# Kernel tuning notes

Measured on AMD Instinct MI355X. Metric: run time of the kernel, lower is better.

Reference implementation:

```python
import jax, jax.numpy as jnp
import numpy as np

N_NODES = 100000
N_EDGES = 1600000
IN_DIM = 128
OUT_DIM = 128


def setup_inputs() -> dict:
    key = jax.random.key(0)
    k1, k2, k3, k4, k5 = jax.random.split(key, 5)
    x = jax.random.normal(k1, (N_NODES, IN_DIM), dtype=jnp.float32)
    edge_src = jax.random.randint(k2, (N_EDGES,), 0, N_NODES, dtype=jnp.int32)
    edge_dst = jax.random.randint(k3, (N_EDGES,), 0, N_NODES, dtype=jnp.int32)
    # nn.Linear(in_dim*2, out_dim): W stored here as [2*in_dim, out_dim] (already transposed)
    W = jax.random.normal(k4, (2 * IN_DIM, OUT_DIM), dtype=jnp.float32) * (1.0 / np.sqrt(2 * IN_DIM))
    b = jax.random.normal(k5, (OUT_DIM,), dtype=jnp.float32) * 0.01
    return {"x": x, "edge_src": edge_src, "edge_dst": edge_dst, "W": W, "b": b}


def reference(x, edge_src, edge_dst, W, b):
    # adj_mean @ x  ==  mean over neighbors: sum_j x[src_j] into row dst_j, / deg(dst)
    n = x.shape[0]
    deg = jax.ops.segment_sum(jnp.ones_like(edge_dst, dtype=x.dtype), edge_dst, num_segments=n)
    deg = jnp.maximum(deg, 1.0)  # rows with no neighbors -> zero vector (0/1)
    neigh = jax.ops.segment_sum(x[edge_src], edge_dst, num_segments=n) / deg[:, None]
    # concat([x, neigh], dim=1) then Linear
    out = jnp.concatenate([x, neigh], axis=1) @ W + b
    return out
```

## Files before the change

### kernel.cpp

```cpp
#include <hip/hip_runtime.h>

#define IN_DIM 128
#define OUT_DIM 128
#define PADCAP 1792
#define EPB 8192

typedef short bf16x8 __attribute__((ext_vector_type(8)));
typedef float f32x4 __attribute__((ext_vector_type(4)));
typedef float f32x2 __attribute__((ext_vector_type(2)));
typedef unsigned int u32x4 __attribute__((ext_vector_type(4)));

__device__ __forceinline__ unsigned short f2bf(float f) {
    union { float f; unsigned int u; } v; v.f = f;
    unsigned int u = v.u;
    u += 0x7FFFu + ((u >> 16) & 1u);
    return (unsigned short)(u >> 16);
}

__global__ __launch_bounds__(256) void prep_kernel(const float* __restrict__ x,
                                                   unsigned char* __restrict__ xq,
                                                   const float* __restrict__ W,
                                                   unsigned short* __restrict__ WF,
                                                   int* __restrict__ cursor,
                                                   int nN, int total8, int nconv, int nb) {
    const int b = blockIdx.x;
    const int t = threadIdx.x;
    if (b < nconv) {
        int i = b * 256 + t;
        if (i >= total8) return;
        const float4* p = (const float4*)x + (size_t)i * 2;
        float4 v0 = p[0], v1 = p[1];
        int w0 = 0, w1 = 0;
        w0 = __builtin_amdgcn_cvt_pk_fp8_f32(v0.x, v0.y, w0, false);
        w0 = __builtin_amdgcn_cvt_pk_fp8_f32(v0.z, v0.w, w0, true);
        w1 = __builtin_amdgcn_cvt_pk_fp8_f32(v1.x, v1.y, w1, false);
        w1 = __builtin_amdgcn_cvt_pk_fp8_f32(v1.z, v1.w, w1, true);
        uint2 o; o.x = (unsigned int)w0; o.y = (unsigned int)w1;
        int node = i >> 4, oct = i & 15;
        int q = oct >> 2, o8 = oct & 3;
        *(uint2*)(xq + (size_t)q * (nN + 1) * 32 + (size_t)node * 32 + o8 * 8) = o;
    } else if (b < nconv + 16) {
        int tt = (b - nconv) * 256 + t;
        int frag = tt >> 6, lane = tt & 63;
        int f = frag >> 3, c = frag & 7;
        int col = c * 16 + (lane & 15);
        int kbase = f * 32 + (lane >> 4) * 8;
        bf16x8 h;
#pragma unroll
        for (int i = 0; i < 8; i++)
            h[i] = (short)f2bf(W[(size_t)(kbase + i) * OUT_DIM + col]);
        *(bf16x8*)(WF + (size_t)tt * 8) = h;
    } else if (b == nconv + 16) {
        if (t < 32) {
            int q = t >> 3, o = t & 7;
            *(unsigned int*)(xq + (size_t)q * (nN + 1) * 32 + (size_t)nN * 32 + o * 4) = 0u;
        }
    } else {
        int i = (b - nconv - 17) * 256 + t;
        if (i < nb) cursor[i] = i * PADCAP;
    }
}

__global__ __launch_bounds__(1024) void place_kernel(const int* __restrict__ src,
                                                     const int* __restrict__ dst,
                                                     int* __restrict__ cursor,
                                                     unsigned int* __restrict__ csr_packed,
                                                     int nE, int nb) {
    __shared__ int lcnt[2048];
    __shared__ int lbase[2048];
    const int t = threadIdx.x;
    for (int i = t; i < nb; i += 1024) lcnt[i] = 0;
    __syncthreads();
    const int e0 = blockIdx.x * EPB;
    unsigned int meta[EPB / 1024];
#pragma unroll
    for (int k = 0; k < EPB / 1024; k++) {
        int e = e0 + k * 1024 + t;
        if (e < nE) {
            int d = dst[e];
            int bk = d >> 6, dl = d & 63;
            int r = atomicAdd(&lcnt[bk], 1);
            meta[k] = ((unsigned)bk << 20) | ((unsigned)dl << 14) | (unsigned)r;
        } else meta[k] = 0xFFFFFFFFu;
    }
    __syncthreads();
    for (int i = t; i < nb; i += 1024) {
        int c = lcnt[i];
        lbase[i] = c ? atomicAdd(&cursor[i], c) : 0;
    }
    __syncthreads();
#pragma unroll
    for (int k = 0; k < EPB / 1024; k++) {
        if (meta[k] != 0xFFFFFFFFu) {
            int e = e0 + k * 1024 + t;
            unsigned int m = meta[k];
            int bk = m >> 20, dl = (m >> 14) & 63, r = m & 0x3FFF;
            csr_packed[lbase[bk] + r] = ((unsigned)dl << 17) | (unsigned)src[e];
        }
    }
}

__global__ __launch_bounds__(256) void sort_kernel(unsigned int* __restrict__ csr_packed,
                                                   int* __restrict__ cursor,
                                                   unsigned int* __restrict__ rowinfo,
                                                   int nN, int nb) {
    __shared__ int bcnt[64];
    __shared__ int bpst[64];
    __shared__ int s_npad;
    __shared__ unsigned int sorted[PADCAP];
    const int b = blockIdx.x;
    const int t = threadIdx.x;
    const int lane = t & 63;
    const int wave = t >> 6;
    const size_t e0 = (size_t)b * PADCAP;
    int n = cursor[b] - (int)(b * PADCAP);
    if (n > PADCAP) n = PADCAP;

    const unsigned int sentinel = (unsigned)nN << 5;
    if (t < 64) bcnt[t] = 0;
#pragma unroll
    for (int k = 0; k < 7; k++) sorted[k * 256 + t] = sentinel;
    __syncthreads();

    unsigned int pk[7]; int rk[7];
#pragma unroll
    for (int k = 0; k < 7; k++) {
        int idx = k * 256 + t;
        if (idx < n) {
            unsigned int p = csr_packed[e0 + idx];
            pk[k] = p;
            rk[k] = atomicAdd(&bcnt[(p >> 17) & 63], 1);
        } else pk[k] = 0xFFFFFFFFu;
    }
    __syncthreads();

    if (wave == 0) {
        int dg = bcnt[lane];
        int pl = (dg + 7) & ~7;
        int s = pl;
#pragma unroll
        for (int off = 1; off < 64; off <<= 1) {
            int u = __shfl_up(s, off);
            if (lane >= off) s += u;
        }
        bpst[lane] = s - pl;
        if (lane == 63) s_npad = s;
        unsigned key = ((unsigned)dg << 6) | (unsigned)lane;
#pragma unroll
        for (int k = 2; k <= 64; k <<= 1) {
#pragma unroll
            for (int j = k >> 1; j > 0; j >>= 1) {
                unsigned other = __shfl_xor(key, j);
                bool lower = (lane & j) == 0;
                bool asc   = (lane & k) == 0;
                unsigned mn = min(key, other), mx = max(key, other);
                key = (lower == asc) ? mn : mx;
            }
        }
        int rowid = key & 63;
        int deg2  = key >> 6;
        rowinfo[b * 64 + lane] = (unsigned)bpst[rowid] | ((unsigned)deg2 << 11)
                               | ((unsigned)rowid << 21);
    }
    __syncthreads();

#pragma unroll
    for (int k = 0; k < 7; k++) {
        if (pk[k] != 0xFFFFFFFFu) {
            int dl = (pk[k] >> 17) & 63;
            sorted[bpst[dl] + rk[k]] = (pk[k] & 0x1FFFFu) << 5;
        }
    }
    __syncthreads();

    const int npadtot = s_npad;
#pragma unroll
    for (int k = 0; k < 7; k++) {
        int idx = k * 256 + t;
        if (idx < npadtot) csr_packed[e0 + idx] = sorted[idx];
    }
    if (t == 0) cursor[b] = npadtot;
}

__global__ __launch_bounds__(256, 8) void qgather_kernel(const unsigned char* __restrict__ xq,
                                                         const unsigned int* __restrict__ csr_packed,
                                                         const unsigned int* __restrict__ rowinfo,
                                                         const int* __restrict__ cursor,
                                                         unsigned short* __restrict__ neigh,
                                                         int nN, int nb) {
    __shared__ unsigned int el[PADCAP];
    __shared__ int bst[64];
    __shared__ int bdg[64];
    __shared__ int brw[64];

    const int bid = blockIdx.x;
    const int xcd = bid & 7;
    const int quarter = xcd & 3;
    const int bucket = (bid >> 3) * 2 + (xcd >> 2);
    if (bucket >= nb) return;

    const int t = threadIdx.x;
    const int lane = t & 63;
    const int wave = t >> 6;

    if (t < 64) {
        unsigned int ri = rowinfo[bucket * 64 + t];
        bst[t] = (int)(ri & 0x7FFu);
        bdg[t] = (int)((ri >> 11) & 0x3FFu);
        brw[t] = (int)((ri >> 21) & 63u);
    }
    __syncthreads();
    const size_t e0 = (size_t)bucket * PADCAP;
    const int npad = cursor[bucket];
    for (int idx = t; idx < npad; idx += 256) el[idx] = csr_packed[e0 + idx];
    __syncthreads();

    const int g = lane >> 2;
    const int c = lane & 3;
    const unsigned char* plane = xq + (size_t)quarter * (nN + 1) * 32 + c * 8;
    const int qoff = quarter * 32;

    const int r  = wave * 16 + g;
    const int st = bst[r];
    const int dg = bdg[r];
    const int pl = (dg + 7) & ~7;
    const unsigned int* ep = el + st;

    f32x2 a0{0.f, 0.f}, a1{0.f, 0.f}, a2{0.f, 0.f}, a3{0.f, 0.f};
    for (int j = 0; j < pl; j += 8) {
#pragma unroll
        for (int u = 0; u < 8; u++) {
            unsigned int s = ep[j + ((u + g) & 7)];
            uint2 v = *(const uint2*)(plane + s);
            f32x2 p;
            p = __builtin_amdgcn_cvt_pk_f32_fp8(v.x, false); a0 += p;
            p = __builtin_amdgcn_cvt_pk_f32_fp8(v.x, true);  a1 += p;
            p = __builtin_amdgcn_cvt_pk_f32_fp8(v.y, false); a2 += p;
            p = __builtin_amdgcn_cvt_pk_f32_fp8(v.y, true);  a3 += p;
        }
    }
    const float rd = 1.0f / (float)((dg > 0) ? dg : 1);
    a0 *= rd; a1 *= rd; a2 *= rd; a3 *= rd;
    unsigned int w0, w1, w2, w3;
    asm("v_cvt_pk_bf16_f32 %0, %1, %2" : "=v"(w0) : "v"(a0.x), "v"(a0.y));
    asm("v_cvt_pk_bf16_f32 %0, %1, %2" : "=v"(w1) : "v"(a1.x), "v"(a1.y));
    asm("v_cvt_pk_bf16_f32 %0, %1, %2" : "=v"(w2) : "v"(a2.x), "v"(a2.y));
    asm("v_cvt_pk_bf16_f32 %0, %1, %2" : "=v"(w3) : "v"(a3.x), "v"(a3.y));
    u32x4 o = {w0, w1, w2, w3};
    const int row = bucket * 64 + brw[r];
    *(u32x4*)(neigh + (size_t)row * IN_DIM + qoff + c * 8) = o;
}

__global__ __launch_bounds__(256, 6) void gemm_kernel(const float* __restrict__ x,
                                                      const unsigned short* __restrict__ neigh,
                                                      const unsigned short* __restrict__ WF,
                                                      const float* __restrict__ bias,
                                                      float* __restrict__ out, int nN) {
    const int t = threadIdx.x;
    const int lane = t & 63;
    const int wave = t >> 6;
    const int row0 = blockIdx.x * 64;

    f32x4 acc[8];
#pragma unroll
    for (int c = 0; c < 8; c++) acc[c] = f32x4{0.f, 0.f, 0.f, 0.f};

    const int arow = wave * 16 + (lane & 15);
    const int koff = (lane >> 4) * 8;
    const int rowc = min(row0 + arow, nN - 1);
    const float*          xrow = x     + (size_t)rowc * IN_DIM;
    const unsigned short* nrow = neigh + (size_t)rowc * IN_DIM;

#pragma unroll
    for (int f = 0; f < 8; f++) {
        bf16x8 af;
        if (f < 4) {
            const float* px = xrow + f * 32 + koff;
            float4 v0 = *(const float4*)px;
            float4 v1 = *(const float4*)(px + 4);
            unsigned int r0, r1, r2, r3;
            asm("v_cvt_pk_bf16_f32 %0, %1, %2" : "=v"(r0) : "v"(v0.x), "v"(v0.y));
            asm("v_cvt_pk_bf16_f32 %0, %1, %2" : "=v"(r1) : "v"(v0.z), "v"(v0.w));
            asm("v_cvt_pk_bf16_f32 %0, %1, %2" : "=v"(r2) : "v"(v1.x), "v"(v1.y));
            asm("v_cvt_pk_bf16_f32 %0, %1, %2" : "=v"(r3) : "v"(v1.z), "v"(v1.w));
            union { unsigned int u[4]; bf16x8 v; } cv;
            cv.u[0] = r0; cv.u[1] = r1; cv.u[2] = r2; cv.u[3] = r3;
            af = cv.v;
        } else {
            af = *(const bf16x8*)(nrow + (f - 4) * 32 + koff);
        }
#pragma unroll
        for (int c = 0; c < 8; c++) {
            bf16x8 bf = *(const bf16x8*)(WF + ((size_t)(f * 8 + c) * 64 + lane) * 8);
            acc[c] = __builtin_amdgcn_mfma_f32_16x16x32_bf16(af, bf, acc[c], 0, 0, 0);
        }
    }

    const int orow0 = row0 + wave * 16 + (lane >> 4) * 4;
    const int ocol  = lane & 15;
#pragma unroll
    for (int c = 0; c < 8; c++) {
        const float bv = bias[c * 16 + ocol];
#pragma unroll
        for (int r = 0; r < 4; r++) {
            int row = orow0 + r;
            if (row < nN)
                out[(size_t)row * OUT_DIM + c * 16 + ocol] = acc[c][r] + bv;
        }
    }
}

extern "C" void kernel_launch(void* const* d_in, const int* in_sizes, int n_in,
                              void* d_out, int out_size, void* d_ws, size_t ws_size,
                              hipStream_t stream) {
    const float* x        = (const float*)d_in[0];
    const int*   edge_src = (const int*)d_in[1];
    const int*   edge_dst = (const int*)d_in[2];
    const float* W        = (const float*)d_in[3];
    const float* bias     = (const float*)d_in[4];
    float* out = (float*)d_out;

    const int nN = in_sizes[0] / IN_DIM;
    const int nE = in_sizes[1];
    const int nb = (nN + 63) >> 6;

    int* cursor = (int*)d_ws;
    unsigned int* csr_packed = (unsigned int*)(cursor + 2048);
    unsigned int* rowinfo = csr_packed + (size_t)nb * PADCAP;
    unsigned char* xq = (unsigned char*)(rowinfo + (size_t)nb * 64);
    unsigned short* WF = (unsigned short*)(xq + (size_t)4 * (nN + 1) * 32);
    unsigned short* neigh = WF + 128 * 256;

    const int total8 = nN * IN_DIM / 8;
    const int nconv  = (total8 + 255) / 256;
    const int ninit  = (nb + 255) / 256;
    prep_kernel<<<nconv + 17 + ninit, 256, 0, stream>>>(x, xq, W, WF, cursor,
                                                        nN, total8, nconv, nb);

    const int eblk = (nE + EPB - 1) / EPB;
    place_kernel<<<eblk, 1024, 0, stream>>>(edge_src, edge_dst, cursor, csr_packed, nE, nb);
    sort_kernel<<<nb, 256, 0, stream>>>(csr_packed, cursor, rowinfo, nN, nb);

    const int nbp2 = (nb + 1) / 2;
    qgather_kernel<<<nbp2 * 8, 256, 0, stream>>>(xq, csr_packed, rowinfo, cursor, neigh, nN, nb);
    gemm_kernel<<<(nN + 63) / 64, 256, 0, stream>>>(x, neigh, WF, bias, out, nN);
}
```

Baseline: 110.0 us.

## Fuse per-bucket counting sort into gather kernel, drop sort kernel and rowinfo

The separate sort kernel, which bucketed edges by destination row, wrote the sorted list and row metadata back to global memory, is removed. Each gather block now redoes that counting sort in shared memory for its bucket before gathering. This saves one kernel launch and a global write/read round trip of the CSR and rowinfo. The cost is that every bucket's sort is done four times, once per quarter block, and the gather blocks need more shared memory and registers, which may lower occupancy.

```diff
diff --git a/kernel.cpp b/kernel.cpp
--- a/kernel.cpp
+++ b/kernel.cpp
@@ -100,26 +100,36 @@
     }
 }
 
-__global__ __launch_bounds__(256) void sort_kernel(unsigned int* __restrict__ csr_packed,
-                                                   int* __restrict__ cursor,
-                                                   unsigned int* __restrict__ rowinfo,
-                                                   int nN, int nb) {
+__global__ __launch_bounds__(256, 8) void qgather_kernel(const unsigned char* __restrict__ xq,
+                                                         const unsigned int* __restrict__ csr_packed,
+                                                         const int* __restrict__ cursor,
+                                                         unsigned short* __restrict__ neigh,
+                                                         int nN, int nb) {
+    __shared__ unsigned int el[PADCAP];
     __shared__ int bcnt[64];
     __shared__ int bpst[64];
-    __shared__ int s_npad;
-    __shared__ unsigned int sorted[PADCAP];
-    const int b = blockIdx.x;
+    __shared__ int bst[64];
+    __shared__ int bdg[64];
+    __shared__ int brw[64];
+
+    const int bid = blockIdx.x;
+    const int xcd = bid & 7;
+    const int quarter = xcd & 3;
+    const int bucket = (bid >> 3) * 2 + (xcd >> 2);
+    if (bucket >= nb) return;
+
     const int t = threadIdx.x;
     const int lane = t & 63;
     const int wave = t >> 6;
-    const size_t e0 = (size_t)b * PADCAP;
-    int n = cursor[b] - (int)(b * PADCAP);
+
+    const size_t e0 = (size_t)bucket * PADCAP;
+    int n = cursor[bucket] - bucket * PADCAP;
     if (n > PADCAP) n = PADCAP;
 
     const unsigned int sentinel = (unsigned)nN << 5;
     if (t < 64) bcnt[t] = 0;
 #pragma unroll
-    for (int k = 0; k < 7; k++) sorted[k * 256 + t] = sentinel;
+    for (int k = 0; k < 7; k++) el[k * 256 + t] = sentinel;
     __syncthreads();
 
     unsigned int pk[7]; int rk[7];
@@ -144,7 +154,6 @@
             if (lane >= off) s += u;
         }
         bpst[lane] = s - pl;
-        if (lane == 63) s_npad = s;
         unsigned key = ((unsigned)dg << 6) | (unsigned)lane;
 #pragma unroll
         for (int k = 2; k <= 64; k <<= 1) {
@@ -158,9 +167,9 @@
             }
         }
         int rowid = key & 63;
-        int deg2  = key >> 6;
-        rowinfo[b * 64 + lane] = (unsigned)bpst[rowid] | ((unsigned)deg2 << 11)
-                               | ((unsigned)rowid << 21);
+        bst[lane] = bpst[rowid];
+        bdg[lane] = (int)(key >> 6);
+        brw[lane] = rowid;
     }
     __syncthreads();
 
@@ -168,51 +177,9 @@
     for (int k = 0; k < 7; k++) {
         if (pk[k] != 0xFFFFFFFFu) {
             int dl = (pk[k] >> 17) & 63;
-            sorted[bpst[dl] + rk[k]] = (pk[k] & 0x1FFFFu) << 5;
-        }
-    }
-    __syncthreads();
-
-    const int npadtot = s_npad;
-#pragma unroll
-    for (int k = 0; k < 7; k++) {
-        int idx = k * 256 + t;
-        if (idx < npadtot) csr_packed[e0 + idx] = sorted[idx];
-    }
-    if (t == 0) cursor[b] = npadtot;
-}
-
-__global__ __launch_bounds__(256, 8) void qgather_kernel(const unsigned char* __restrict__ xq,
-                                                         const unsigned int* __restrict__ csr_packed,
-                                                         const unsigned int* __restrict__ rowinfo,
-                                                         const int* __restrict__ cursor,
-                                                         unsigned short* __restrict__ neigh,
-                                                         int nN, int nb) {
-    __shared__ unsigned int el[PADCAP];
-    __shared__ int bst[64];
-    __shared__ int bdg[64];
-    __shared__ int brw[64];
-
-    const int bid = blockIdx.x;
-    const int xcd = bid & 7;
-    const int quarter = xcd & 3;
-    const int bucket = (bid >> 3) * 2 + (xcd >> 2);
-    if (bucket >= nb) return;
-
-    const int t = threadIdx.x;
-    const int lane = t & 63;
-    const int wave = t >> 6;
-
-    if (t < 64) {
-        unsigned int ri = rowinfo[bucket * 64 + t];
-        bst[t] = (int)(ri & 0x7FFu);
-        bdg[t] = (int)((ri >> 11) & 0x3FFu);
-        brw[t] = (int)((ri >> 21) & 63u);
-    }
-    __syncthreads();
-    const size_t e0 = (size_t)bucket * PADCAP;
-    const int npad = cursor[bucket];
-    for (int idx = t; idx < npad; idx += 256) el[idx] = csr_packed[e0 + idx];
+            el[bpst[dl] + rk[k]] = (pk[k] & 0x1FFFFu) << 5;
+        }
+    }
     __syncthreads();
 
     const int g = lane >> 2;
@@ -326,8 +293,7 @@
 
     int* cursor = (int*)d_ws;
     unsigned int* csr_packed = (unsigned int*)(cursor + 2048);
-    unsigned int* rowinfo = csr_packed + (size_t)nb * PADCAP;
-    unsigned char* xq = (unsigned char*)(rowinfo + (size_t)nb * 64);
+    unsigned char* xq = (unsigned char*)(csr_packed + (size_t)nb * PADCAP);
     unsigned short* WF = (unsigned short*)(xq + (size_t)4 * (nN + 1) * 32);
     unsigned short* neigh = WF + 128 * 256;
 
@@ -339,9 +305,8 @@
 
     const int eblk = (nE + EPB - 1) / EPB;
     place_kernel<<<eblk, 1024, 0, stream>>>(edge_src, edge_dst, cursor, csr_packed, nE, nb);
-    sort_kernel<<<nb, 256, 0, stream>>>(csr_packed, cursor, rowinfo, nN, nb);
 
     const int nbp2 = (nb + 1) / 2;
-    qgather_kernel<<<nbp2 * 8, 256, 0, stream>>>(xq, csr_packed, rowinfo, cursor, neigh, nN, nb);
+    qgather_kernel<<<nbp2 * 8, 256, 0, stream>>>(xq, csr_packed, cursor, neigh, nN, nb);
     gemm_kernel<<<(nN + 63) / 64, 256, 0, stream>>>(x, neigh, WF, bias, out, nN);
 }
```

Result: faster. 107.6 us (-2.2%).
